# Performance work log

Hardware: AMD Instinct MI355X
Metric: run time of the kernel (lower is better)

The kernel has to match this reference:

```python
import jax, jax.numpy as jnp
import numpy as np

N, M, D = 8192, 2048, 32


def setup_inputs() -> dict:
    key = jax.random.key(0)
    k1, k2, k3 = jax.random.split(key, 3)
    samples = jax.random.normal(k1, (N, D), dtype=jnp.float32)
    means = jax.random.normal(k2, (M, D), dtype=jnp.float32)
    # stds are divisors; keep them strictly positive, in [0.5, 1.5)
    stds = jax.random.uniform(k3, (M, D), dtype=jnp.float32) + 0.5
    return {"samples": samples, "means": means, "stds": stds}


def reference(samples, means, stds):
    # [N, M, D] broadcast pairwise weighted squared distance (full-buffer KDE)
    diff = means[None, :, :] - samples[:, None, :]
    logp = -0.5 * jnp.sum(jnp.square(diff) / stds[None, :, :], axis=2)  # [N, M]
    dist = jnp.mean(jnp.exp(logp), axis=1)  # [N]
    # invert=True branch: flip the density around its midrange
    dist = -dist + jnp.max(dist) + jnp.min(dist)
    return dist
```

## Files before the change

### kernel.cpp

```cpp
#include <hip/hip_runtime.h>

#define NS 8192
#define MS 2048
#define DD 32
#define MSPLIT 32
#define MCH (MS / MSPLIT)
#define NITS (MCH / 16)

typedef __attribute__((ext_vector_type(8))) short bf16x8;
typedef __attribute__((ext_vector_type(4))) float f32x4;
typedef unsigned short u16;
typedef unsigned int u32;

#define PART_OFF 0
#define DIST_OFF (MSPLIT * NS * 4)
#define MM_OFF   (DIST_OFF + NS * 4)

__device__ inline float fast_exp2(float x) {
#if __has_builtin(__builtin_amdgcn_exp2f)
    return __builtin_amdgcn_exp2f(x);
#else
    return exp2f(x);
#endif
}

__device__ inline u32 cvt_pk_bf16(float a, float b) {
    u32 r;
    asm("v_cvt_pk_bf16_f32 %0, %1, %2" : "=v"(r) : "v"(a), "v"(b));
    return r;
}

__device__ inline void split8(const float* v, bf16x8& hi, bf16x8& lo) {
    union { u32 u[4]; bf16x8 b; } H, L;
#pragma unroll
    for (int j = 0; j < 4; ++j) {
        u32 h = cvt_pk_bf16(v[2 * j], v[2 * j + 1]);
        float ha = __uint_as_float(h << 16);
        float hb = __uint_as_float(h & 0xFFFF0000u);
        L.u[j] = cvt_pk_bf16(v[2 * j] - ha, v[2 * j + 1] - hb);
        H.u[j] = h;
    }
    hi = H.b;
    lo = L.b;
}

__global__ __launch_bounds__(256, 4) void kde_fused(const float* __restrict__ samples,
                                                    const float* __restrict__ means,
                                                    const float* __restrict__ stds,
                                                    unsigned char* __restrict__ wsb) {
    __shared__ u16 WBH[NITS * 4 * 16 * 8];
    __shared__ u16 WBL[NITS * 4 * 16 * 8];
    __shared__ u16 WCH[NITS * 4 * 16 * 8];
    __shared__ u16 WCL[NITS * 4 * 16 * 8];
    __shared__ float A2s[MCH];

    const int t = threadIdx.x;
    const int m0 = blockIdx.y * MCH;
    const float L2E = 1.4426950408889634f;

    if (blockIdx.x == 0 && blockIdx.y == 0 && t == 0) {
        unsigned* mm = (unsigned*)(wsb + MM_OFF);
        mm[0] = 0x7f7fffffu;
        mm[1] = 0u;
    }

    {
        const int ml = t >> 2, qd = t & 3;
        const float* mp = means + (size_t)(m0 + ml) * DD + qd * 8;
        const float* vp = stds  + (size_t)(m0 + ml) * DD + qd * 8;
        float4 a4 = *(const float4*)mp, b4 = *(const float4*)(mp + 4);
        float4 c4 = *(const float4*)vp, d4 = *(const float4*)(vp + 4);
        float mu[8] = {a4.x, a4.y, a4.z, a4.w, b4.x, b4.y, b4.z, b4.w};
        float sd[8] = {c4.x, c4.y, c4.z, c4.w, d4.x, d4.y, d4.z, d4.w};
        float Bv[8], Cv[8], a = 0.f;
#pragma unroll
        for (int j = 0; j < 8; ++j) {
            float inv = 1.0f / sd[j];
            Bv[j] = L2E * mu[j] * inv;
            Cv[j] = -0.5f * L2E * inv;
            a += mu[j] * mu[j] * inv;
        }
        a += __shfl_xor(a, 1);
        a += __shfl_xor(a, 2);
        if (qd == 0) A2s[ml] = -0.5f * L2E * a - 11.0f;

        bf16x8 bh, bl, ch, cl;
        split8(Bv, bh, bl);
        split8(Cv, ch, cl);
        const int it = ml >> 4, r15 = ml & 15;
        const int base = ((it * 4 + qd) * 16 + r15) * 8;
        *(bf16x8*)&WBH[base] = bh;
        *(bf16x8*)&WBL[base] = bl;
        *(bf16x8*)&WCH[base] = ch;
        *(bf16x8*)&WCL[base] = cl;
    }

    const int lane = t & 63, wid = t >> 6;
    const int r15 = lane & 15, g = lane >> 4;
    const int n0 = blockIdx.x * 256 + wid * 64;

    bf16x8 xh[4], xl[4], qh[4], ql[4];
#pragma unroll
    for (int nt = 0; nt < 4; ++nt) {
        const float* sp = samples + (size_t)(n0 + nt * 16 + r15) * DD + g * 8;
        float4 a4 = *(const float4*)sp, b4 = *(const float4*)(sp + 4);
        float xv[8] = {a4.x, a4.y, a4.z, a4.w, b4.x, b4.y, b4.z, b4.w};
        float qv[8];
#pragma unroll
        for (int j = 0; j < 8; ++j) qv[j] = xv[j] * xv[j];
        split8(xv, xh[nt], xl[nt]);
        split8(qv, qh[nt], ql[nt]);
    }

    __syncthreads();

    f32x4 rs[4];
#pragma unroll
    for (int nt = 0; nt < 4; ++nt) rs[nt] = (f32x4){0.f, 0.f, 0.f, 0.f};

#pragma unroll 2
    for (int it = 0; it < NITS; ++it) {
        const int base = ((it * 4 + g) * 16 + r15) * 8;
        bf16x8 bh = *(const bf16x8*)&WBH[base];
        bf16x8 ch = *(const bf16x8*)&WCH[base];
        bf16x8 bl = *(const bf16x8*)&WBL[base];
        bf16x8 cl = *(const bf16x8*)&WCL[base];
        const float a2 = A2s[it * 16 + r15];
#pragma unroll
        for (int nt = 0; nt < 4; ++nt) {
            f32x4 accB = (f32x4){0.f, 0.f, 0.f, 0.f};
            f32x4 accC = (f32x4){0.f, 0.f, 0.f, 0.f};
            accB = __builtin_amdgcn_mfma_f32_16x16x32_bf16(xh[nt], bh, accB, 0, 0, 0);
            accC = __builtin_amdgcn_mfma_f32_16x16x32_bf16(qh[nt], ch, accC, 0, 0, 0);
            accB = __builtin_amdgcn_mfma_f32_16x16x32_bf16(xl[nt], bh, accB, 0, 0, 0);
            accC = __builtin_amdgcn_mfma_f32_16x16x32_bf16(ql[nt], ch, accC, 0, 0, 0);
            accB = __builtin_amdgcn_mfma_f32_16x16x32_bf16(xh[nt], bl, accB, 0, 0, 0);
            accC = __builtin_amdgcn_mfma_f32_16x16x32_bf16(qh[nt], cl, accC, 0, 0, 0);
#pragma unroll
            for (int r = 0; r < 4; ++r)
                rs[nt][r] += fast_exp2((accB[r] + accC[r]) + a2);
        }
    }

#pragma unroll
    for (int o = 1; o < 16; o <<= 1)
#pragma unroll
        for (int nt = 0; nt < 4; ++nt)
#pragma unroll
            for (int r = 0; r < 4; ++r) rs[nt][r] += __shfl_xor(rs[nt][r], o);

    float* partial = (float*)(wsb + PART_OFF);
    if (r15 == 0) {
#pragma unroll
        for (int nt = 0; nt < 4; ++nt)
            *(f32x4*)(partial + (size_t)blockIdx.y * NS + n0 + nt * 16 + g * 4) = rs[nt];
    }
}

__global__ __launch_bounds__(256) void reduce_mm(const unsigned char* __restrict__ wsb,
                                                 float* __restrict__ dist,
                                                 unsigned* __restrict__ mm) {
    const float* partial = (const float*)(wsb + PART_OFF);
    const int tid = threadIdx.x;
    const int n = blockIdx.x * 256 + tid;
    float v = 0.f;
#pragma unroll
    for (int j = 0; j < MSPLIT; ++j) v += partial[(size_t)j * NS + n];
    dist[n] = v;

    float mn = v, mx = v;
#pragma unroll
    for (int o = 1; o < 64; o <<= 1) {
        mn = fminf(mn, __shfl_xor(mn, o));
        mx = fmaxf(mx, __shfl_xor(mx, o));
    }
    __shared__ float smn[4], smx[4];
    const int wv = tid >> 6, ln = tid & 63;
    if (ln == 0) { smn[wv] = mn; smx[wv] = mx; }
    __syncthreads();
    if (tid == 0) {
#pragma unroll
        for (int j = 1; j < 4; ++j) {
            mn = fminf(mn, smn[j]);
            mx = fmaxf(mx, smx[j]);
        }
        atomicMin(mm + 0, __float_as_uint(mn));
        atomicMax(mm + 1, __float_as_uint(mx));
    }
}

__global__ __launch_bounds__(256) void finalize(const float* __restrict__ dist,
                                                const unsigned* __restrict__ mm,
                                                float* __restrict__ out) {
    const int i = blockIdx.x * 256 + threadIdx.x;
    const float fmn = __uint_as_float(mm[0]);
    const float fmx = __uint_as_float(mm[1]);
    f32x4 d = ((const f32x4*)dist)[i];
    f32x4 o;
#pragma unroll
    for (int r = 0; r < 4; ++r) o[r] = fmx + fmn - d[r];
    ((f32x4*)out)[i] = o;
}

extern "C" void kernel_launch(void* const* d_in, const int* in_sizes, int n_in,
                              void* d_out, int out_size, void* d_ws, size_t ws_size,
                              hipStream_t stream) {
    const float* samples = (const float*)d_in[0];
    const float* means   = (const float*)d_in[1];
    const float* stds    = (const float*)d_in[2];
    unsigned char* ws = (unsigned char*)d_ws;
    float* out = (float*)d_out;

    float* dist = (float*)(ws + DIST_OFF);
    unsigned* mm = (unsigned*)(ws + MM_OFF);

    kde_fused<<<dim3(NS / 256, MSPLIT), 256, 0, stream>>>(samples, means, stds, ws);
    reduce_mm<<<dim3(NS / 256), 256, 0, stream>>>(ws, dist, mm);
    finalize<<<dim3(NS / 4 / 256), 256, 0, stream>>>(dist, mm, out);
}
```

Before: 19.47 us.

## Precompute bf16 splits in a prep kernel and load them into swizzled LDS

```diff
diff --git a/kernel.cpp b/kernel.cpp
--- a/kernel.cpp
+++ b/kernel.cpp
@@ -4,17 +4,26 @@
 #define MS 2048
 #define DD 32
 #define MSPLIT 32
-#define MCH (MS / MSPLIT)
-#define NITS (MCH / 16)
+#define MCH 64
+#define NITS 4
 
 typedef __attribute__((ext_vector_type(8))) short bf16x8;
 typedef __attribute__((ext_vector_type(4))) float f32x4;
 typedef unsigned short u16;
 typedef unsigned int u32;
 
-#define PART_OFF 0
-#define DIST_OFF (MSPLIT * NS * 4)
-#define MM_OFF   (DIST_OFF + NS * 4)
+#define WBH_OFF  0
+#define WBL_OFF  (WBH_OFF + MS*32*2)
+#define WCH_OFF  (WBL_OFF + MS*32*2)
+#define WCL_OFF  (WCH_OFF + MS*32*2)
+#define XH_OFF   (WCL_OFF + MS*32*2)
+#define XL_OFF   (XH_OFF + NS*DD*2)
+#define QH_OFF   (XL_OFF + NS*DD*2)
+#define QL_OFF   (QH_OFF + NS*DD*2)
+#define A2_OFF   (QL_OFF + NS*DD*2)
+#define PART_OFF (A2_OFF + MS*4)
+#define DIST_OFF (PART_OFF + MSPLIT*NS*4)
+#define MM_OFF   (DIST_OFF + NS*4)
 
 __device__ inline float fast_exp2(float x) {
 #if __has_builtin(__builtin_amdgcn_exp2f)
@@ -44,55 +53,93 @@
     lo = L.b;
 }
 
-__global__ __launch_bounds__(256, 4) void kde_fused(const float* __restrict__ samples,
-                                                    const float* __restrict__ means,
-                                                    const float* __restrict__ stds,
-                                                    unsigned char* __restrict__ wsb) {
-    __shared__ u16 WBH[NITS * 4 * 16 * 8];
-    __shared__ u16 WBL[NITS * 4 * 16 * 8];
-    __shared__ u16 WCH[NITS * 4 * 16 * 8];
-    __shared__ u16 WCL[NITS * 4 * 16 * 8];
-    __shared__ float A2s[MCH];
-
-    const int t = threadIdx.x;
-    const int m0 = blockIdx.y * MCH;
-    const float L2E = 1.4426950408889634f;
-
-    if (blockIdx.x == 0 && blockIdx.y == 0 && t == 0) {
-        unsigned* mm = (unsigned*)(wsb + MM_OFF);
+__global__ __launch_bounds__(256) void prep(const float* __restrict__ samples,
+                                            const float* __restrict__ means,
+                                            const float* __restrict__ stds,
+                                            unsigned char* __restrict__ ws) {
+    const int tid = threadIdx.x, bid = blockIdx.x;
+    if (bid == 0 && tid == 0) {
+        unsigned* mm = (unsigned*)(ws + MM_OFF);
         mm[0] = 0x7f7fffffu;
         mm[1] = 0u;
     }
-
-    {
-        const int ml = t >> 2, qd = t & 3;
-        const float* mp = means + (size_t)(m0 + ml) * DD + qd * 8;
-        const float* vp = stds  + (size_t)(m0 + ml) * DD + qd * 8;
+    const float L2E = 1.4426950408889634f;
+    if (bid < 64) {
+        const int p = bid * 256 + tid;
+        const int m = p >> 3;
+        const int c = p & 7;
+        const int g = c & 3;
+        const bool isB = (c < 4);
+
+        const float* mp = means + (size_t)m * DD + g * 8;
+        const float* vp = stds  + (size_t)m * DD + g * 8;
         float4 a4 = *(const float4*)mp, b4 = *(const float4*)(mp + 4);
         float4 c4 = *(const float4*)vp, d4 = *(const float4*)(vp + 4);
         float mu[8] = {a4.x, a4.y, a4.z, a4.w, b4.x, b4.y, b4.z, b4.w};
         float sd[8] = {c4.x, c4.y, c4.z, c4.w, d4.x, d4.y, d4.z, d4.w};
-        float Bv[8], Cv[8], a = 0.f;
+        float val[8], a = 0.f;
 #pragma unroll
         for (int j = 0; j < 8; ++j) {
             float inv = 1.0f / sd[j];
-            Bv[j] = L2E * mu[j] * inv;
-            Cv[j] = -0.5f * L2E * inv;
-            a += mu[j] * mu[j] * inv;
+            val[j] = isB ? (L2E * mu[j] * inv) : (-0.5f * L2E * inv);
+            if (isB) a += mu[j] * mu[j] * inv;
         }
         a += __shfl_xor(a, 1);
         a += __shfl_xor(a, 2);
-        if (qd == 0) A2s[ml] = -0.5f * L2E * a - 11.0f;
-
-        bf16x8 bh, bl, ch, cl;
-        split8(Bv, bh, bl);
-        split8(Cv, ch, cl);
-        const int it = ml >> 4, r15 = ml & 15;
-        const int base = ((it * 4 + qd) * 16 + r15) * 8;
-        *(bf16x8*)&WBH[base] = bh;
-        *(bf16x8*)&WBL[base] = bl;
-        *(bf16x8*)&WCH[base] = ch;
-        *(bf16x8*)&WCL[base] = cl;
+        a += __shfl_xor(a, 4);
+        if (c == 0) ((float*)(ws + A2_OFF))[m] = -0.5f * L2E * a - 11.0f;
+
+        bf16x8 hi, lo;
+        split8(val, hi, lo);
+        const size_t idx = (size_t)((m >> 4) * 4 + g) * 128 + (m & 15) * 8;
+        u16* WH = (u16*)(ws + (isB ? WBH_OFF : WCH_OFF));
+        u16* WL = (u16*)(ws + (isB ? WBL_OFF : WCL_OFF));
+        *(bf16x8*)(WH + idx) = hi;
+        *(bf16x8*)(WL + idx) = lo;
+    } else {
+        const int idx = (bid - 64) * 256 + tid;
+        float4 v = ((const float4*)samples)[idx];
+        float xv[4] = {v.x, v.y, v.z, v.w};
+        float qv[4];
+#pragma unroll
+        for (int j = 0; j < 4; ++j) qv[j] = xv[j] * xv[j];
+        union { u32 u[2]; ushort4 s; } HX, LX, HQ, LQ;
+#pragma unroll
+        for (int j = 0; j < 2; ++j) {
+            u32 h = cvt_pk_bf16(xv[2 * j], xv[2 * j + 1]);
+            float ha = __uint_as_float(h << 16);
+            float hb = __uint_as_float(h & 0xFFFF0000u);
+            LX.u[j] = cvt_pk_bf16(xv[2 * j] - ha, xv[2 * j + 1] - hb);
+            HX.u[j] = h;
+            h = cvt_pk_bf16(qv[2 * j], qv[2 * j + 1]);
+            ha = __uint_as_float(h << 16);
+            hb = __uint_as_float(h & 0xFFFF0000u);
+            LQ.u[j] = cvt_pk_bf16(qv[2 * j] - ha, qv[2 * j + 1] - hb);
+            HQ.u[j] = h;
+        }
+        *(ushort4*)((u16*)(ws + XH_OFF) + idx * 4) = HX.s;
+        *(ushort4*)((u16*)(ws + XL_OFF) + idx * 4) = LX.s;
+        *(ushort4*)((u16*)(ws + QH_OFF) + idx * 4) = HQ.s;
+        *(ushort4*)((u16*)(ws + QL_OFF) + idx * 4) = LQ.s;
+    }
+}
+
+__global__ __launch_bounds__(256, 4) void kde_mfma(const unsigned char* __restrict__ ws,
+                                                   float* __restrict__ partial) {
+    __shared__ u16 LBH[2048], LBL[2048], LCH[2048], LCL[2048];
+    __shared__ float A2s[MCH];
+
+    const int t = threadIdx.x;
+    const int mb = blockIdx.y;
+
+    {
+        const u32 src = mb * 2048 + t * 8;
+        const u32 dst = (t * 16) ^ (((t >> 4) & 3) << 5);
+        *(bf16x8*)((char*)LBH + dst) = *(const bf16x8*)((const u16*)(ws + WBH_OFF) + src);
+        *(bf16x8*)((char*)LBL + dst) = *(const bf16x8*)((const u16*)(ws + WBL_OFF) + src);
+        *(bf16x8*)((char*)LCH + dst) = *(const bf16x8*)((const u16*)(ws + WCH_OFF) + src);
+        *(bf16x8*)((char*)LCL + dst) = *(const bf16x8*)((const u16*)(ws + WCL_OFF) + src);
+        if (t < MCH) A2s[t] = ((const float*)(ws + A2_OFF))[mb * MCH + t];
     }
 
     const int lane = t & 63, wid = t >> 6;
@@ -102,14 +149,11 @@
     bf16x8 xh[4], xl[4], qh[4], ql[4];
 #pragma unroll
     for (int nt = 0; nt < 4; ++nt) {
-        const float* sp = samples + (size_t)(n0 + nt * 16 + r15) * DD + g * 8;
-        float4 a4 = *(const float4*)sp, b4 = *(const float4*)(sp + 4);
-        float xv[8] = {a4.x, a4.y, a4.z, a4.w, b4.x, b4.y, b4.z, b4.w};
-        float qv[8];
-#pragma unroll
-        for (int j = 0; j < 8; ++j) qv[j] = xv[j] * xv[j];
-        split8(xv, xh[nt], xl[nt]);
-        split8(qv, qh[nt], ql[nt]);
+        const size_t off = (size_t)(n0 + nt * 16 + r15) * DD + g * 8;
+        xh[nt] = *(const bf16x8*)((const u16*)(ws + XH_OFF) + off);
+        xl[nt] = *(const bf16x8*)((const u16*)(ws + XL_OFF) + off);
+        qh[nt] = *(const bf16x8*)((const u16*)(ws + QH_OFF) + off);
+        ql[nt] = *(const bf16x8*)((const u16*)(ws + QL_OFF) + off);
     }
 
     __syncthreads();
@@ -117,28 +161,28 @@
     f32x4 rs[4];
 #pragma unroll
     for (int nt = 0; nt < 4; ++nt) rs[nt] = (f32x4){0.f, 0.f, 0.f, 0.f};
+
+    const u32 wbase = ((u32)((g * 16 + r15) * 16)) ^ (g << 5);
 
 #pragma unroll 2
     for (int it = 0; it < NITS; ++it) {
-        const int base = ((it * 4 + g) * 16 + r15) * 8;
-        bf16x8 bh = *(const bf16x8*)&WBH[base];
-        bf16x8 ch = *(const bf16x8*)&WCH[base];
-        bf16x8 bl = *(const bf16x8*)&WBL[base];
-        bf16x8 cl = *(const bf16x8*)&WCL[base];
+        const u32 b = wbase + it * 1024;
+        bf16x8 bh = *(const bf16x8*)((const char*)LBH + b);
+        bf16x8 ch = *(const bf16x8*)((const char*)LCH + b);
+        bf16x8 bl = *(const bf16x8*)((const char*)LBL + b);
+        bf16x8 cl = *(const bf16x8*)((const char*)LCL + b);
         const float a2 = A2s[it * 16 + r15];
 #pragma unroll
         for (int nt = 0; nt < 4; ++nt) {
-            f32x4 accB = (f32x4){0.f, 0.f, 0.f, 0.f};
-            f32x4 accC = (f32x4){0.f, 0.f, 0.f, 0.f};
-            accB = __builtin_amdgcn_mfma_f32_16x16x32_bf16(xh[nt], bh, accB, 0, 0, 0);
-            accC = __builtin_amdgcn_mfma_f32_16x16x32_bf16(qh[nt], ch, accC, 0, 0, 0);
-            accB = __builtin_amdgcn_mfma_f32_16x16x32_bf16(xl[nt], bh, accB, 0, 0, 0);
-            accC = __builtin_amdgcn_mfma_f32_16x16x32_bf16(ql[nt], ch, accC, 0, 0, 0);
-            accB = __builtin_amdgcn_mfma_f32_16x16x32_bf16(xh[nt], bl, accB, 0, 0, 0);
-            accC = __builtin_amdgcn_mfma_f32_16x16x32_bf16(qh[nt], cl, accC, 0, 0, 0);
-#pragma unroll
-            for (int r = 0; r < 4; ++r)
-                rs[nt][r] += fast_exp2((accB[r] + accC[r]) + a2);
+            f32x4 acc = (f32x4){a2, a2, a2, a2};
+            acc = __builtin_amdgcn_mfma_f32_16x16x32_bf16(xh[nt], bh, acc, 0, 0, 0);
+            acc = __builtin_amdgcn_mfma_f32_16x16x32_bf16(qh[nt], ch, acc, 0, 0, 0);
+            acc = __builtin_amdgcn_mfma_f32_16x16x32_bf16(xl[nt], bh, acc, 0, 0, 0);
+            acc = __builtin_amdgcn_mfma_f32_16x16x32_bf16(ql[nt], ch, acc, 0, 0, 0);
+            acc = __builtin_amdgcn_mfma_f32_16x16x32_bf16(xh[nt], bl, acc, 0, 0, 0);
+            acc = __builtin_amdgcn_mfma_f32_16x16x32_bf16(qh[nt], cl, acc, 0, 0, 0);
+#pragma unroll
+            for (int r = 0; r < 4; ++r) rs[nt][r] += fast_exp2(acc[r]);
         }
     }
 
@@ -149,11 +193,10 @@
 #pragma unroll
             for (int r = 0; r < 4; ++r) rs[nt][r] += __shfl_xor(rs[nt][r], o);
 
-    float* partial = (float*)(wsb + PART_OFF);
     if (r15 == 0) {
 #pragma unroll
         for (int nt = 0; nt < 4; ++nt)
-            *(f32x4*)(partial + (size_t)blockIdx.y * NS + n0 + nt * 16 + g * 4) = rs[nt];
+            *(f32x4*)(partial + (size_t)mb * NS + n0 + nt * 16 + g * 4) = rs[nt];
     }
 }
 
@@ -214,7 +257,8 @@
     float* dist = (float*)(ws + DIST_OFF);
     unsigned* mm = (unsigned*)(ws + MM_OFF);
 
-    kde_fused<<<dim3(NS / 256, MSPLIT), 256, 0, stream>>>(samples, means, stds, ws);
+    prep<<<dim3(64 + NS * DD / 4 / 256), 256, 0, stream>>>(samples, means, stds, ws);
+    kde_mfma<<<dim3(NS / 256, MSPLIT), 256, 0, stream>>>(ws, (float*)(ws + PART_OFF));
     reduce_mm<<<dim3(NS / 256), 256, 0, stream>>>(ws, dist, mm);
     finalize<<<dim3(NS / 4 / 256), 256, 0, stream>>>(dist, mm, out);
 }
```

Result: slower. 23.56 us (+21.0%).
